# Kernel tuning notes

Hardware: AMD Instinct MI355X
Metric: run time of the kernel (lower is better)

## Reference

```python
import jax, jax.numpy as jnp
import numpy as np

B, L, H = 2, 2048, 1024
E = H * 2          # mamba_dim = model_dim * expansion_factor
K = 4              # conv kernel size
N = 16             # SSM state dim
DT_RANK = H // 8   # 128, mamba default ceil(d_model/16) scaled on d_inner


def setup_inputs() -> dict:
    key = jax.random.key(0)
    ks = jax.random.split(key, 12)
    s = lambda fan_in: 1.0 / np.sqrt(fan_in)
    return {
        "x": jax.random.normal(ks[0], (B, L, H), jnp.float32),
        "W_in": jax.random.normal(ks[1], (H, 2 * E), jnp.float32) * s(H),
        "b_in": jnp.zeros((2 * E,), jnp.float32),
        "conv_w": jax.random.normal(ks[2], (E, 1, K), jnp.float32) * s(K),  # depthwise OIH
        "conv_b": jnp.zeros((E,), jnp.float32),
        "x_proj_w": jax.random.normal(ks[3], (E, DT_RANK + 2 * N), jnp.float32) * s(E),
        "dt_proj_w": jax.random.normal(ks[4], (DT_RANK, E), jnp.float32) * s(DT_RANK),
        "dt_bias": jax.random.uniform(ks[5], (E,), jnp.float32, -4.0, -2.0),  # softplus(.) small
        "A_log": jnp.log(jnp.broadcast_to(jnp.arange(1, N + 1, dtype=jnp.float32), (E, N))),
        "D_param": jnp.ones((E,), jnp.float32),
        "W_out": jax.random.normal(ks[6], (E, H), jnp.float32) * s(E),
        "b_out": jnp.zeros((H,), jnp.float32),
    }


def _selective_scan(u, delta, A, Bm, Cm, Dp):
    # u, delta: (B,L,E); A: (E,N); Bm, Cm: (B,L,N); Dp: (E,)
    def step(h, inp):
        d_t, u_t, b_t, c_t = inp          # (B,E), (B,E), (B,N), (B,N)
        dA = jnp.exp(d_t[..., None] * A)  # (B,E,N)
        h = dA * h + (d_t * u_t)[..., None] * b_t[:, None, :]
        y = jnp.einsum("ben,bn->be", h, c_t)
        return h, y

    h0 = jnp.zeros((u.shape[0], A.shape[0], A.shape[1]), u.dtype)
    xs = (delta.transpose(1, 0, 2), u.transpose(1, 0, 2),
          Bm.transpose(1, 0, 2), Cm.transpose(1, 0, 2))
    _, ys = jax.lax.scan(step, h0, xs)    # ys: (L,B,E)
    return ys.transpose(1, 0, 2) + u * Dp


def reference(x, W_in, b_in, conv_w, conv_b, x_proj_w, dt_proj_w, dt_bias,
              A_log, D_param, W_out, b_out):
    silu = jax.nn.silu
    z = x @ W_in + b_in                    # (B,L,2E)
    xc, xr = z[..., :E], z[..., E:]
    xr = silu(xr)
    # causal depthwise conv1d: left-pad K-1 (== torch pad=K-1 then truncate to L)
    xt = xc.transpose(0, 2, 1)             # (B,E,L)
    xt = jax.lax.conv_general_dilated(
        xt, conv_w, window_strides=(1,), padding=[(K - 1, 0)],
        feature_group_count=E, dimension_numbers=("NCH", "OIH", "NCH"))
    xc = silu((xt + conv_b[None, :, None]).transpose(0, 2, 1))  # (B,L,E)
    # S6 selective SSM
    proj = xc @ x_proj_w                   # (B,L,dt_rank+2N)
    dt = proj[..., :DT_RANK]
    Bm = proj[..., DT_RANK:DT_RANK + N]
    Cm = proj[..., DT_RANK + N:]
    delta = jax.nn.softplus(dt @ dt_proj_w + dt_bias)  # (B,L,E)
    A = -jnp.exp(A_log)                    # (E,N)
    y = _selective_scan(xc, delta, A, Bm, Cm, D_param)
    y = y * xr                             # gate
    return y @ W_out + b_out
```

## Files before the change

kernel.cpp:

```cpp
#include <hip/hip_runtime.h>
#include <cstdint>

#define SL 2048
#define SE 2048
#define SB 2
#define SN 16
#define SC 64
#define ST 32

enum { EP_SPLIT_SILU = 1, EP_SOFTPLUS = 2, EP_BIAS = 3, EP_PARTIAL = 4 };

typedef __attribute__((ext_vector_type(8))) short bf16x8;
typedef __attribute__((ext_vector_type(4))) float f32x4;

__device__ __forceinline__ float silu_f(float x) { return x / (1.f + __expf(-x)); }
__device__ __forceinline__ float softplus_f(float x) {
    return (x > 20.f) ? x : log1pf(__expf(x));
}
__device__ __forceinline__ ushort f2bf(float f) {
    union { float f; unsigned u; } a; a.f = f;
    unsigned r = a.u + 0x7fff + ((a.u >> 16) & 1);
    return (ushort)(r >> 16);
}
__device__ __forceinline__ void gload16(const void* g, void* l) {
    __builtin_amdgcn_global_load_lds(
        (const __attribute__((address_space(1))) unsigned int*)g,
        (__attribute__((address_space(3))) unsigned int*)l, 16, 0, 0);
}

template <int MODE>
__global__ __launch_bounds__(512, 2) void hgemm256(
    const ushort* __restrict__ A, const ushort* __restrict__ Bt,
    float* __restrict__ C, const float* __restrict__ bias,
    float* __restrict__ out2, int M, int N, int K, int Esplit, int KS)
{
    __shared__ ushort As[2][256 * 32];
    __shared__ ushort Bs[2][256 * 32];
    const int tid = threadIdx.x;
    const int w = tid >> 6, l = tid & 63;
    const int wr = w >> 2, wc = w & 3;
    const int m0 = blockIdx.y * 256, n0 = blockIdx.x * 256;
    const int z = blockIdx.z;
    const int kbeg = z * KS;
    const int nt = KS / 32;
    const int srow = l >> 2;
    const int scol = (l & 3) * 8;

    f32x4 acc[8][4];
#pragma unroll
    for (int m = 0; m < 8; m++)
#pragma unroll
        for (int n = 0; n < 4; n++) acc[m][n] = (f32x4)(0.f);

    auto stage = [&](int buf, int t) {
        const int k0 = kbeg + t * 32;
#pragma unroll
        for (int r = 0; r < 2; r++) {
            const int row = w * 32 + r * 16 + srow;
            gload16(A + (size_t)(m0 + row) * K + k0 + scol,
                    &As[buf][(w * 32 + r * 16) * 32]);
            gload16(Bt + (size_t)(n0 + row) * K + k0 + scol,
                    &Bs[buf][(w * 32 + r * 16) * 32]);
        }
    };

    stage(0, 0);
    __syncthreads();

    int cur = 0;
    const int fr = l & 15, kc = (l >> 4) * 8;
    for (int t = 0; t < nt; t++) {
        if (t + 1 < nt) stage(cur ^ 1, t + 1);
        bf16x8 af[8], bfr[4];
#pragma unroll
        for (int m = 0; m < 8; m++)
            af[m] = *(const bf16x8*)&As[cur][(wr * 128 + m * 16 + fr) * 32 + kc];
#pragma unroll
        for (int n = 0; n < 4; n++)
            bfr[n] = *(const bf16x8*)&Bs[cur][(wc * 64 + n * 16 + fr) * 32 + kc];
#pragma unroll
        for (int m = 0; m < 8; m++)
#pragma unroll
            for (int n = 0; n < 4; n++)
                acc[m][n] = __builtin_amdgcn_mfma_f32_16x16x32_bf16(
                    af[m], bfr[n], acc[m][n], 0, 0, 0);
        __syncthreads();
        cur ^= 1;
    }

    const int cr = (l >> 4) * 4, cc = l & 15;
    float* pbase = C + (size_t)z * M * N;
#pragma unroll
    for (int m = 0; m < 8; m++) {
#pragma unroll
        for (int j = 0; j < 4; j++) {
            const int row = m0 + wr * 128 + m * 16 + cr + j;
#pragma unroll
            for (int n = 0; n < 4; n++) {
                const int col = n0 + wc * 64 + n * 16 + cc;
                float v = acc[m][n][j];
                if (MODE == EP_SPLIT_SILU) {
                    v += bias[col];
                    if (col < Esplit)
                        C[(size_t)row * Esplit + col] = v;
                    else
                        out2[(size_t)row * Esplit + (col - Esplit)] = silu_f(v);
                } else if (MODE == EP_BIAS) {
                    C[(size_t)row * N + col] = v + bias[col];
                } else {
                    pbase[(size_t)row * N + col] = v;
                }
            }
        }
    }
}

template <int MODE>
__global__ __launch_bounds__(256, 2) void hgemm2(
    const ushort* __restrict__ A, const ushort* __restrict__ Bt,
    float* __restrict__ C, const float* __restrict__ bias,
    float* __restrict__ out2, int M, int N, int K, int Esplit, int KS)
{
    __shared__ ushort As[2][128 * 64];
    __shared__ ushort Bs[2][128 * 64];
    const int tid = threadIdx.x;
    const int w = tid >> 6, l = tid & 63;
    const int wr = w >> 1, wc = w & 1;
    const int m0 = blockIdx.y * 128, n0 = blockIdx.x * 128;
    const int z = blockIdx.z;
    const int kbeg = z * KS;
    const int nt = KS / 64;
    const int srow = l >> 3, scol = (l & 7) * 8;

    f32x4 acc[4][4];
#pragma unroll
    for (int m = 0; m < 4; m++)
#pragma unroll
        for (int n = 0; n < 4; n++) acc[m][n] = (f32x4)(0.f);

    auto stage = [&](int buf, int t) {
        const int k0 = kbeg + t * 64;
#pragma unroll
        for (int r = 0; r < 4; r++) {
            const int row = r * 32 + w * 8 + srow;
            int brow = n0 + row; if (brow > N - 1) brow = N - 1;
            gload16(A + (size_t)(m0 + row) * K + k0 + scol,
                    &As[buf][r * 2048 + w * 512]);
            gload16(Bt + (size_t)brow * K + k0 + scol,
                    &Bs[buf][r * 2048 + w * 512]);
        }
    };

    stage(0, 0);
    __syncthreads();

    int cur = 0;
    const int fr = l & 15, kc = (l >> 4) * 8;
    for (int t = 0; t < nt; t++) {
        if (t + 1 < nt) stage(cur ^ 1, t + 1);
#pragma unroll
        for (int kk = 0; kk < 64; kk += 32) {
            bf16x8 af[4], bfr[4];
#pragma unroll
            for (int m = 0; m < 4; m++)
                af[m] = *(const bf16x8*)&As[cur][(wr * 64 + m * 16 + fr) * 64 + kk + kc];
#pragma unroll
            for (int n = 0; n < 4; n++)
                bfr[n] = *(const bf16x8*)&Bs[cur][(wc * 64 + n * 16 + fr) * 64 + kk + kc];
#pragma unroll
            for (int m = 0; m < 4; m++)
#pragma unroll
                for (int n = 0; n < 4; n++)
                    acc[m][n] = __builtin_amdgcn_mfma_f32_16x16x32_bf16(
                        af[m], bfr[n], acc[m][n], 0, 0, 0);
        }
        __syncthreads();
        cur ^= 1;
    }

    const int cr = (l >> 4) * 4, cc = l & 15;
    float* pbase = C + (size_t)z * M * N;
#pragma unroll
    for (int m = 0; m < 4; m++) {
#pragma unroll
        for (int j = 0; j < 4; j++) {
            const int row = m0 + wr * 64 + m * 16 + cr + j;
#pragma unroll
            for (int n = 0; n < 4; n++) {
                const int col = n0 + wc * 64 + n * 16 + cc;
                float v = acc[m][n][j];
                if (MODE == EP_SOFTPLUS) {
                    C[(size_t)row * N + col] = softplus_f(v + bias[col]);
                } else if (MODE == EP_BIAS) {
                    C[(size_t)row * N + col] = v + bias[col];
                } else {
                    if (col < N) pbase[(size_t)row * N + col] = v;
                }
            }
        }
    }
}

__global__ __launch_bounds__(256) void gemm3_reduce(
    const float* __restrict__ Pp, float* __restrict__ proj,
    ushort* __restrict__ dtbf, int M, int N, int Z)
{
    const size_t g = (size_t)blockIdx.x * 256 + threadIdx.x;
    const size_t tot = (size_t)M * N;
    if (g >= tot) return;
    float s = 0.f;
    for (int z = 0; z < Z; z++) s += Pp[(size_t)z * tot + g];
    proj[g] = s;
    const int col = (int)(g % N);
    if (col < 128) {
        const size_t row = g / N;
        dtbf[row * 128 + col] = f2bf(s);
    }
}

__global__ __launch_bounds__(256) void reduce6(
    const float* __restrict__ Pp, const float* __restrict__ bias,
    float* __restrict__ out, int M, int N, int Z)
{
    const size_t g = (size_t)blockIdx.x * 256 + threadIdx.x;
    const size_t tot4 = (size_t)M * N / 4;
    if (g >= tot4) return;
    const int n4 = N / 4;
    float4 s = ((const float4*)bias)[g % n4];
    for (int z = 0; z < Z; z++) {
        float4 p = ((const float4*)Pp)[z * tot4 + g];
        s.x += p.x; s.y += p.y; s.z += p.z; s.w += p.w;
    }
    ((float4*)out)[g] = s;
}

__global__ __launch_bounds__(256) void f2bf_vec(
    const float* __restrict__ in, ushort* __restrict__ out, size_t n4)
{
    for (size_t i = (size_t)blockIdx.x * 256 + threadIdx.x; i < n4;
         i += (size_t)gridDim.x * 256) {
        float4 v = ((const float4*)in)[i];
        ushort4 o;
        o.x = f2bf(v.x); o.y = f2bf(v.y); o.z = f2bf(v.z); o.w = f2bf(v.w);
        ((ushort4*)out)[i] = o;
    }
}

__global__ __launch_bounds__(256) void f2bf_transpose(
    const float* __restrict__ W, ushort* __restrict__ Wt, int R, int Ccols)
{
    __shared__ float tile[32][33];
    const int bc = blockIdx.x * 32, br = blockIdx.y * 32;
    const int tx = threadIdx.x & 31, ty = threadIdx.x >> 5;
    for (int i = ty; i < 32; i += 8)
        tile[i][tx] = W[(size_t)(br + i) * Ccols + bc + tx];
    __syncthreads();
    for (int i = ty; i < 32; i += 8)
        Wt[(size_t)(bc + i) * R + br + tx] = f2bf(tile[tx][i]);
}

__global__ __launch_bounds__(256) void conv_silu4(
    const float* __restrict__ xin, const float* __restrict__ w,
    const float* __restrict__ cb, float* __restrict__ xo,
    ushort* __restrict__ xobf, int Ln, int En, size_t total4)
{
    const int Eq = En >> 2;
    for (size_t idx = (size_t)blockIdx.x * 256 + threadIdx.x; idx < total4;
         idx += (size_t)gridDim.x * 256) {
        const int e4 = (int)(idx % Eq);
        const size_t row = idx / Eq;
        const int l = (int)(row % Ln);
        float4 acc = ((const float4*)cb)[e4];
        const float4 w0 = ((const float4*)w)[e4 * 4 + 0];
        const float4 w1 = ((const float4*)w)[e4 * 4 + 1];
        const float4 w2 = ((const float4*)w)[e4 * 4 + 2];
        const float4 w3 = ((const float4*)w)[e4 * 4 + 3];
        const float wt0[4] = {w0.x, w0.y, w0.z, w0.w};
        const float wt1[4] = {w1.x, w1.y, w1.z, w1.w};
        const float wt2[4] = {w2.x, w2.y, w2.z, w2.w};
        const float wt3[4] = {w3.x, w3.y, w3.z, w3.w};
#pragma unroll
        for (int k = 0; k < 4; k++) {
            if (l - 3 + k >= 0) {
                float4 xv = ((const float4*)xin)[(row - 3 + k) * Eq + e4];
                acc.x = fmaf(wt0[k], xv.x, acc.x);
                acc.y = fmaf(wt1[k], xv.y, acc.y);
                acc.z = fmaf(wt2[k], xv.z, acc.z);
                acc.w = fmaf(wt3[k], xv.w, acc.w);
            }
        }
        float4 v;
        v.x = silu_f(acc.x); v.y = silu_f(acc.y);
        v.z = silu_f(acc.z); v.w = silu_f(acc.w);
        ((float4*)xo)[idx] = v;
        ushort4 o;
        o.x = f2bf(v.x); o.y = f2bf(v.y); o.z = f2bf(v.z); o.w = f2bf(v.w);
        ((ushort4*)xobf)[idx] = o;
    }
}

__global__ __launch_bounds__(256) void scan_pass1(
    const float* __restrict__ delta, const float* __restrict__ u,
    const float* __restrict__ proj, const float* __restrict__ A_log,
    float* __restrict__ Pbuf, float* __restrict__ Sbuf)
{
    __shared__ float sB[ST * SN];
    const int tid = threadIdx.x;
    const int eb = blockIdx.x & 7;
    const int c  = (blockIdx.x >> 3) & (SC - 1);
    const int b  = blockIdx.x >> 9;
    const int e  = eb * 256 + tid;
    const size_t row0 = (size_t)b * SL + c * ST;

    for (int i = tid; i < ST * SN; i += 256) {
        const int tl = i >> 4, n = i & 15;
        sB[i] = proj[(row0 + tl) * 160 + 128 + n];
    }
    __syncthreads();

    float An[SN], h[SN];
    {
        const float4* Ap = (const float4*)(A_log + (size_t)e * SN);
#pragma unroll
        for (int q = 0; q < 4; q++) {
            float4 v = Ap[q];
            An[q * 4 + 0] = -expf(v.x);
            An[q * 4 + 1] = -expf(v.y);
            An[q * 4 + 2] = -expf(v.z);
            An[q * 4 + 3] = -expf(v.w);
        }
    }
#pragma unroll
    for (int n = 0; n < SN; n++) h[n] = 0.f;

    float dsum = 0.f;
    size_t idx = row0 * SE + e;
    float d = delta[idx], uu = u[idx];
    for (int tl = 0; tl < ST; tl++) {
        float dn = 0.f, un = 0.f;
        if (tl + 1 < ST) { dn = delta[idx + SE]; un = u[idx + SE]; }
        const float du = d * uu;
        dsum += d;
#pragma unroll
        for (int n = 0; n < SN; n++) {
            const float dA = __expf(d * An[n]);
            h[n] = fmaf(dA, h[n], du * sB[tl * SN + n]);
        }
        d = dn; uu = un; idx += SE;
    }

    const size_t ob = ((((size_t)c * SB) + b) * SE + e) * SN;
#pragma unroll
    for (int q = 0; q < 4; q++) {
        float4 pv, sv;
        pv.x = __expf(An[q * 4 + 0] * dsum); sv.x = h[q * 4 + 0];
        pv.y = __expf(An[q * 4 + 1] * dsum); sv.y = h[q * 4 + 1];
        pv.z = __expf(An[q * 4 + 2] * dsum); sv.z = h[q * 4 + 2];
        pv.w = __expf(An[q * 4 + 3] * dsum); sv.w = h[q * 4 + 3];
        *(float4*)(Pbuf + ob + q * 4) = pv;
        *(float4*)(Sbuf + ob + q * 4) = sv;
    }
}

__global__ __launch_bounds__(256) void scan_pass2(
    const float* __restrict__ Pbuf, const float* __restrict__ Sbuf,
    float* __restrict__ hinit)
{
    const size_t g = (size_t)blockIdx.x * 256 + threadIdx.x;
    const size_t stride = (size_t)SB * SE * SN;
    float h = 0.f;
    float P = Pbuf[g], S = Sbuf[g];
    for (int c = 0; c < SC; c++) {
        float Pn = 0.f, Sn = 0.f;
        if (c + 1 < SC) {
            Pn = Pbuf[(c + 1) * stride + g];
            Sn = Sbuf[(c + 1) * stride + g];
        }
        hinit[c * stride + g] = h;
        h = fmaf(P, h, S);
        P = Pn; S = Sn;
    }
}

__global__ __launch_bounds__(256) void scan_pass3(
    const float* __restrict__ delta, const float* __restrict__ u,
    const float* __restrict__ proj, const float* __restrict__ A_log,
    const float* __restrict__ Dp, const float* __restrict__ xr,
    const float* __restrict__ hinit, ushort* __restrict__ yg)
{
    __shared__ float sB[ST * SN];
    __shared__ float sC[ST * SN];
    const int tid = threadIdx.x;
    const int eb = blockIdx.x & 7;
    const int c  = (blockIdx.x >> 3) & (SC - 1);
    const int b  = blockIdx.x >> 9;
    const int e  = eb * 256 + tid;
    const size_t row0 = (size_t)b * SL + c * ST;

    for (int i = tid; i < ST * SN; i += 256) {
        const int tl = i >> 4, n = i & 15;
        sB[i] = proj[(row0 + tl) * 160 + 128 + n];
        sC[i] = proj[(row0 + tl) * 160 + 144 + n];
    }
    __syncthreads();

    float An[SN], h[SN];
    {
        const float4* Ap = (const float4*)(A_log + (size_t)e * SN);
#pragma unroll
        for (int q = 0; q < 4; q++) {
            float4 v = Ap[q];
            An[q * 4 + 0] = -expf(v.x);
            An[q * 4 + 1] = -expf(v.y);
            An[q * 4 + 2] = -expf(v.z);
            An[q * 4 + 3] = -expf(v.w);
        }
    }
    {
        const size_t ib = ((((size_t)c * SB) + b) * SE + e) * SN;
#pragma unroll
        for (int q = 0; q < 4; q++) {
            float4 v = *(const float4*)(hinit + ib + q * 4);
            h[q * 4 + 0] = v.x; h[q * 4 + 1] = v.y;
            h[q * 4 + 2] = v.z; h[q * 4 + 3] = v.w;
        }
    }
    const float De = Dp[e];

    size_t idx = row0 * SE + e;
    float d = delta[idx], uu = u[idx], g = xr[idx];
    for (int tl = 0; tl < ST; tl++) {
        float dn = 0.f, un = 0.f, gn = 0.f;
        if (tl + 1 < ST) {
            dn = delta[idx + SE]; un = u[idx + SE]; gn = xr[idx + SE];
        }
        const float du = d * uu;
        float y = 0.f;
#pragma unroll
        for (int n = 0; n < SN; n++) {
            const float dA = __expf(d * An[n]);
            h[n] = fmaf(dA, h[n], du * sB[tl * SN + n]);
            y = fmaf(h[n], sC[tl * SN + n], y);
        }
        yg[idx] = f2bf((y + uu * De) * g);
        d = dn; uu = un; g = gn; idx += SE;
    }
}

extern "C" void kernel_launch(void* const* d_in, const int* in_sizes, int n_in,
                              void* d_out, int out_size, void* d_ws, size_t ws_size,
                              hipStream_t stream)
{
    const int Bc = 2, Lc = 2048, Hc = 1024, Ec = 2048;
    const int M = Bc * Lc;
    const int PN = 160;
    const int SKZ = 8;
    const int SK6 = 4;

    const float* x        = (const float*)d_in[0];
    const float* W_in     = (const float*)d_in[1];
    const float* b_in     = (const float*)d_in[2];
    const float* conv_w   = (const float*)d_in[3];
    const float* conv_b   = (const float*)d_in[4];
    const float* x_proj_w = (const float*)d_in[5];
    const float* dt_proj_w= (const float*)d_in[6];
    const float* dt_bias  = (const float*)d_in[7];
    const float* A_log    = (const float*)d_in[8];
    const float* D_param  = (const float*)d_in[9];
    const float* W_out    = (const float*)d_in[10];
    const float* b_out    = (const float*)d_in[11];
    float* out = (float*)d_out;

    float* ws = (float*)d_ws;
    const size_t ME = (size_t)M * Ec;
    const size_t PS = (size_t)SB * SE * SC * SN;

    float* xc_raw = ws;
    float* xr     = xc_raw + ME;
    float* xc     = xr + ME;
    float* delta  = xc + ME;
    float* proj   = delta + ME;
    float* hinit  = proj + (size_t)M * PN;

    ushort* xbf    = (ushort*)delta;
    ushort* W_in_t = (ushort*)xc;
    ushort* xc_bf  = (ushort*)delta;
    float*  Pp3    = xc_raw;
    ushort* xpw_t  = (ushort*)hinit;
    ushort* dtw_t  = (ushort*)hinit + 327680;
    ushort* dtbf   = (ushort*)hinit + 327680 + 262144;
    float*  Pbuf   = xc_raw;
    float*  Sbuf   = xc_raw + PS;
    ushort* ygbf   = (ushort*)xc_raw;
    ushort* W_out_t= (ushort*)delta;
    float*  Pp6    = xr;

    f2bf_vec<<<1024, 256, 0, stream>>>(x, xbf, (size_t)M * Hc / 4);
    f2bf_transpose<<<dim3(2 * Ec / 32, Hc / 32), 256, 0, stream>>>(
        W_in, W_in_t, Hc, 2 * Ec);
    f2bf_transpose<<<dim3(PN / 32, Ec / 32), 256, 0, stream>>>(
        x_proj_w, xpw_t, Ec, PN);
    f2bf_transpose<<<dim3(Ec / 32, 128 / 32), 256, 0, stream>>>(
        dt_proj_w, dtw_t, 128, Ec);

    hgemm256<EP_SPLIT_SILU><<<dim3(2 * Ec / 256, M / 256, 1), 512, 0, stream>>>(
        xbf, W_in_t, xc_raw, b_in, xr, M, 2 * Ec, Hc, Ec, Hc);

    conv_silu4<<<2048, 256, 0, stream>>>(
        xc_raw, conv_w, conv_b, xc, xc_bf, Lc, Ec, ME / 4);

    hgemm2<EP_PARTIAL><<<dim3(2, M / 128, SKZ), 256, 0, stream>>>(
        xc_bf, xpw_t, Pp3, nullptr, nullptr, M, PN, Ec, 0, Ec / SKZ);
    gemm3_reduce<<<(M * PN + 255) / 256, 256, 0, stream>>>(
        Pp3, proj, dtbf, M, PN, SKZ);

    hgemm2<EP_SOFTPLUS><<<dim3(Ec / 128, M / 128, 1), 256, 0, stream>>>(
        dtbf, dtw_t, delta, dt_bias, nullptr, M, Ec, 128, 0, 128);

    scan_pass1<<<SB * SC * (SE / 256), 256, 0, stream>>>(
        delta, xc, proj, A_log, Pbuf, Sbuf);
    scan_pass2<<<(SB * SE * SN) / 256, 256, 0, stream>>>(Pbuf, Sbuf, hinit);
    scan_pass3<<<SB * SC * (SE / 256), 256, 0, stream>>>(
        delta, xc, proj, A_log, D_param, xr, hinit, ygbf);

    f2bf_transpose<<<dim3(Hc / 32, Ec / 32), 256, 0, stream>>>(
        W_out, W_out_t, Ec, Hc);

    hgemm256<EP_PARTIAL><<<dim3(Hc / 256, M / 256, SK6), 512, 0, stream>>>(
        ygbf, W_out_t, Pp6, nullptr, nullptr, M, Hc, Ec, 0, Ec / SK6);
    reduce6<<<(int)((size_t)M * Hc / 4 + 255) / 256, 256, 0, stream>>>(
        Pp6, b_out, out, M, Hc, SK6);
}
```

Before: 368.2 us.

## Switch big GEMMs to 128x128x64 tiles and specialize the dt_proj GEMM

Replaces the 256x256 tile GEMM used for the input and output projections with a shared 128x128x64 body that has 256 threads per block. It also adds a dedicated single-buffered kernel for the K=128 dt_proj GEMM with the softplus epilogue, and halves the split-K factor for the output projection. Smaller tiles give more blocks for occupancy across the CUs, at the cost of more global and LDS traffic per FLOP than the 256-wide tiles. Separate kernels per GEMM allow per-call specialization.

```diff
diff --git a/kernel.cpp b/kernel.cpp
--- a/kernel.cpp
+++ b/kernel.cpp
@@ -29,38 +29,38 @@
 }
 
 template <int MODE>
-__global__ __launch_bounds__(512, 2) void hgemm256(
+__device__ __forceinline__ void gemm_body(
     const ushort* __restrict__ A, const ushort* __restrict__ Bt,
     float* __restrict__ C, const float* __restrict__ bias,
     float* __restrict__ out2, int M, int N, int K, int Esplit, int KS)
 {
-    __shared__ ushort As[2][256 * 32];
-    __shared__ ushort Bs[2][256 * 32];
+    __shared__ ushort As[2][128 * 64];
+    __shared__ ushort Bs[2][128 * 64];
     const int tid = threadIdx.x;
     const int w = tid >> 6, l = tid & 63;
-    const int wr = w >> 2, wc = w & 3;
-    const int m0 = blockIdx.y * 256, n0 = blockIdx.x * 256;
+    const int wr = w >> 1, wc = w & 1;
+    const int m0 = blockIdx.y * 128, n0 = blockIdx.x * 128;
     const int z = blockIdx.z;
     const int kbeg = z * KS;
-    const int nt = KS / 32;
-    const int srow = l >> 2;
-    const int scol = (l & 3) * 8;
-
-    f32x4 acc[8][4];
-#pragma unroll
-    for (int m = 0; m < 8; m++)
+    const int nt = KS / 64;
+    const int srow = l >> 3, scol = (l & 7) * 8;
+
+    f32x4 acc[4][4];
+#pragma unroll
+    for (int m = 0; m < 4; m++)
 #pragma unroll
         for (int n = 0; n < 4; n++) acc[m][n] = (f32x4)(0.f);
 
     auto stage = [&](int buf, int t) {
-        const int k0 = kbeg + t * 32;
-#pragma unroll
-        for (int r = 0; r < 2; r++) {
-            const int row = w * 32 + r * 16 + srow;
+        const int k0 = kbeg + t * 64;
+#pragma unroll
+        for (int r = 0; r < 4; r++) {
+            const int row = r * 32 + w * 8 + srow;
+            int brow = n0 + row; if (brow > N - 1) brow = N - 1;
             gload16(A + (size_t)(m0 + row) * K + k0 + scol,
-                    &As[buf][(w * 32 + r * 16) * 32]);
-            gload16(Bt + (size_t)(n0 + row) * K + k0 + scol,
-                    &Bs[buf][(w * 32 + r * 16) * 32]);
+                    &As[buf][r * 2048 + w * 512]);
+            gload16(Bt + (size_t)brow * K + k0 + scol,
+                    &Bs[buf][r * 2048 + w * 512]);
         }
     };
 
@@ -71,19 +71,22 @@
     const int fr = l & 15, kc = (l >> 4) * 8;
     for (int t = 0; t < nt; t++) {
         if (t + 1 < nt) stage(cur ^ 1, t + 1);
-        bf16x8 af[8], bfr[4];
-#pragma unroll
-        for (int m = 0; m < 8; m++)
-            af[m] = *(const bf16x8*)&As[cur][(wr * 128 + m * 16 + fr) * 32 + kc];
-#pragma unroll
-        for (int n = 0; n < 4; n++)
-            bfr[n] = *(const bf16x8*)&Bs[cur][(wc * 64 + n * 16 + fr) * 32 + kc];
-#pragma unroll
-        for (int m = 0; m < 8; m++)
+#pragma unroll
+        for (int kk = 0; kk < 64; kk += 32) {
+            bf16x8 af[4], bfr[4];
+#pragma unroll
+            for (int m = 0; m < 4; m++)
+                af[m] = *(const bf16x8*)&As[cur][(wr * 64 + m * 16 + fr) * 64 + kk + kc];
 #pragma unroll
             for (int n = 0; n < 4; n++)
-                acc[m][n] = __builtin_amdgcn_mfma_f32_16x16x32_bf16(
-                    af[m], bfr[n], acc[m][n], 0, 0, 0);
+                bfr[n] = *(const bf16x8*)&Bs[cur][(wc * 64 + n * 16 + fr) * 64 + kk + kc];
+#pragma unroll
+            for (int m = 0; m < 4; m++)
+#pragma unroll
+                for (int n = 0; n < 4; n++)
+                    acc[m][n] = __builtin_amdgcn_mfma_f32_16x16x32_bf16(
+                        af[m], bfr[n], acc[m][n], 0, 0, 0);
+        }
         __syncthreads();
         cur ^= 1;
     }
@@ -91,10 +94,10 @@
     const int cr = (l >> 4) * 4, cc = l & 15;
     float* pbase = C + (size_t)z * M * N;
 #pragma unroll
-    for (int m = 0; m < 8; m++) {
+    for (int m = 0; m < 4; m++) {
 #pragma unroll
         for (int j = 0; j < 4; j++) {
-            const int row = m0 + wr * 128 + m * 16 + cr + j;
+            const int row = m0 + wr * 64 + m * 16 + cr + j;
 #pragma unroll
             for (int n = 0; n < 4; n++) {
                 const int col = n0 + wc * 64 + n * 16 + cc;
@@ -108,29 +111,41 @@
                 } else if (MODE == EP_BIAS) {
                     C[(size_t)row * N + col] = v + bias[col];
                 } else {
-                    pbase[(size_t)row * N + col] = v;
+                    if (col < N) pbase[(size_t)row * N + col] = v;
                 }
             }
         }
     }
 }
 
-template <int MODE>
-__global__ __launch_bounds__(256, 2) void hgemm2(
+__global__ __launch_bounds__(256, 2) void g1_gemm(
     const ushort* __restrict__ A, const ushort* __restrict__ Bt,
     float* __restrict__ C, const float* __restrict__ bias,
     float* __restrict__ out2, int M, int N, int K, int Esplit, int KS)
-{
-    __shared__ ushort As[2][128 * 64];
-    __shared__ ushort Bs[2][128 * 64];
+{ gemm_body<EP_SPLIT_SILU>(A, Bt, C, bias, out2, M, N, K, Esplit, KS); }
+
+__global__ __launch_bounds__(256, 2) void g3_gemm(
+    const ushort* __restrict__ A, const ushort* __restrict__ Bt,
+    float* __restrict__ C, int M, int N, int K, int KS)
+{ gemm_body<EP_PARTIAL>(A, Bt, C, nullptr, nullptr, M, N, K, 0, KS); }
+
+__global__ __launch_bounds__(256, 2) void g6_gemm(
+    const ushort* __restrict__ A, const ushort* __restrict__ Bt,
+    float* __restrict__ C, int M, int N, int K, int KS)
+{ gemm_body<EP_PARTIAL>(A, Bt, C, nullptr, nullptr, M, N, K, 0, KS); }
+
+__global__ __launch_bounds__(256) void g4_gemm(
+    const ushort* __restrict__ A, const ushort* __restrict__ Bt,
+    float* __restrict__ C, const float* __restrict__ bias, int M, int N)
+{
+    __shared__ ushort As[128 * 64];
+    __shared__ ushort Bs[128 * 64];
     const int tid = threadIdx.x;
     const int w = tid >> 6, l = tid & 63;
     const int wr = w >> 1, wc = w & 1;
     const int m0 = blockIdx.y * 128, n0 = blockIdx.x * 128;
-    const int z = blockIdx.z;
-    const int kbeg = z * KS;
-    const int nt = KS / 64;
     const int srow = l >> 3, scol = (l & 7) * 8;
+    const int K = 128;
 
     f32x4 acc[4][4];
 #pragma unroll
@@ -138,35 +153,26 @@
 #pragma unroll
         for (int n = 0; n < 4; n++) acc[m][n] = (f32x4)(0.f);
 
-    auto stage = [&](int buf, int t) {
-        const int k0 = kbeg + t * 64;
+    const int fr = l & 15, kc = (l >> 4) * 8;
+#pragma unroll
+    for (int t = 0; t < 2; t++) {
+        const int k0 = t * 64;
 #pragma unroll
         for (int r = 0; r < 4; r++) {
             const int row = r * 32 + w * 8 + srow;
-            int brow = n0 + row; if (brow > N - 1) brow = N - 1;
-            gload16(A + (size_t)(m0 + row) * K + k0 + scol,
-                    &As[buf][r * 2048 + w * 512]);
-            gload16(Bt + (size_t)brow * K + k0 + scol,
-                    &Bs[buf][r * 2048 + w * 512]);
-        }
-    };
-
-    stage(0, 0);
-    __syncthreads();
-
-    int cur = 0;
-    const int fr = l & 15, kc = (l >> 4) * 8;
-    for (int t = 0; t < nt; t++) {
-        if (t + 1 < nt) stage(cur ^ 1, t + 1);
+            gload16(A + (size_t)(m0 + row) * K + k0 + scol, &As[r * 2048 + w * 512]);
+            gload16(Bt + (size_t)(n0 + row) * K + k0 + scol, &Bs[r * 2048 + w * 512]);
+        }
+        __syncthreads();
 #pragma unroll
         for (int kk = 0; kk < 64; kk += 32) {
             bf16x8 af[4], bfr[4];
 #pragma unroll
             for (int m = 0; m < 4; m++)
-                af[m] = *(const bf16x8*)&As[cur][(wr * 64 + m * 16 + fr) * 64 + kk + kc];
+                af[m] = *(const bf16x8*)&As[(wr * 64 + m * 16 + fr) * 64 + kk + kc];
 #pragma unroll
             for (int n = 0; n < 4; n++)
-                bfr[n] = *(const bf16x8*)&Bs[cur][(wc * 64 + n * 16 + fr) * 64 + kk + kc];
+                bfr[n] = *(const bf16x8*)&Bs[(wc * 64 + n * 16 + fr) * 64 + kk + kc];
 #pragma unroll
             for (int m = 0; m < 4; m++)
 #pragma unroll
@@ -175,11 +181,9 @@
                         af[m], bfr[n], acc[m][n], 0, 0, 0);
         }
         __syncthreads();
-        cur ^= 1;
     }
 
     const int cr = (l >> 4) * 4, cc = l & 15;
-    float* pbase = C + (size_t)z * M * N;
 #pragma unroll
     for (int m = 0; m < 4; m++) {
 #pragma unroll
@@ -188,14 +192,7 @@
 #pragma unroll
             for (int n = 0; n < 4; n++) {
                 const int col = n0 + wc * 64 + n * 16 + cc;
-                float v = acc[m][n][j];
-                if (MODE == EP_SOFTPLUS) {
-                    C[(size_t)row * N + col] = softplus_f(v + bias[col]);
-                } else if (MODE == EP_BIAS) {
-                    C[(size_t)row * N + col] = v + bias[col];
-                } else {
-                    if (col < N) pbase[(size_t)row * N + col] = v;
-                }
+                C[(size_t)row * N + col] = softplus_f(acc[m][n][j] + bias[col]);
             }
         }
     }
@@ -455,7 +452,7 @@
     const int M = Bc * Lc;
     const int PN = 160;
     const int SKZ = 8;
-    const int SK6 = 4;
+    const int SK6 = 2;
 
     const float* x        = (const float*)d_in[0];
     const float* W_in     = (const float*)d_in[1];
@@ -503,19 +500,19 @@
     f2bf_transpose<<<dim3(Ec / 32, 128 / 32), 256, 0, stream>>>(
         dt_proj_w, dtw_t, 128, Ec);
 
-    hgemm256<EP_SPLIT_SILU><<<dim3(2 * Ec / 256, M / 256, 1), 512, 0, stream>>>(
+    g1_gemm<<<dim3(2 * Ec / 128, M / 128, 1), 256, 0, stream>>>(
         xbf, W_in_t, xc_raw, b_in, xr, M, 2 * Ec, Hc, Ec, Hc);
 
     conv_silu4<<<2048, 256, 0, stream>>>(
         xc_raw, conv_w, conv_b, xc, xc_bf, Lc, Ec, ME / 4);
 
-    hgemm2<EP_PARTIAL><<<dim3(2, M / 128, SKZ), 256, 0, stream>>>(
-        xc_bf, xpw_t, Pp3, nullptr, nullptr, M, PN, Ec, 0, Ec / SKZ);
+    g3_gemm<<<dim3(2, M / 128, SKZ), 256, 0, stream>>>(
+        xc_bf, xpw_t, Pp3, M, PN, Ec, Ec / SKZ);
     gemm3_reduce<<<(M * PN + 255) / 256, 256, 0, stream>>>(
         Pp3, proj, dtbf, M, PN, SKZ);
 
-    hgemm2<EP_SOFTPLUS><<<dim3(Ec / 128, M / 128, 1), 256, 0, stream>>>(
-        dtbf, dtw_t, delta, dt_bias, nullptr, M, Ec, 128, 0, 128);
+    g4_gemm<<<dim3(Ec / 128, M / 128), 256, 0, stream>>>(
+        dtbf, dtw_t, delta, dt_bias, M, Ec);
 
     scan_pass1<<<SB * SC * (SE / 256), 256, 0, stream>>>(
         delta, xc, proj, A_log, Pbuf, Sbuf);
@@ -526,8 +523,8 @@
     f2bf_transpose<<<dim3(Hc / 32, Ec / 32), 256, 0, stream>>>(
         W_out, W_out_t, Ec, Hc);
 
-    hgemm256<EP_PARTIAL><<<dim3(Hc / 256, M / 256, SK6), 512, 0, stream>>>(
-        ygbf, W_out_t, Pp6, nullptr, nullptr, M, Hc, Ec, 0, Ec / SK6);
+    g6_gemm<<<dim3(Hc / 128, M / 128, SK6), 256, 0, stream>>>(
+        ygbf, W_out_t, Pp6, M, Hc, Ec, Ec / SK6);
     reduce6<<<(int)((size_t)M * Hc / 4 + 255) / 256, 256, 0, stream>>>(
         Pp6, b_out, out, M, Hc, SK6);
 }
```

After: 360.9 us. -2.0%, faster.
